# Kernel tuning notes

Measured on AMD Instinct MI355X. Metric: run time of the kernel, lower is better.

The kernel has to match this reference:

```python
import jax, jax.numpy as jnp
import numpy as np

# Dimensions
T = 1024      # tokens
D = 1024      # d_model
DFF = 1024    # expert intermediate dim
R = 64        # tucker rank (r_in == r_out)
G = 8         # n_group
E = 32        # experts_per_group
NEXP = G * E  # 256 routed experts
K = 8         # top-k


def setup_inputs() -> dict:
    key = jax.random.key(0)
    ks = jax.random.split(key, 12)
    s = 0.02
    return {
        "x": jax.random.normal(ks[0], (T, D), jnp.float32),
        "Wg": jax.random.normal(ks[1], (D, NEXP), jnp.float32) * s,
        "uin_gate": jax.random.normal(ks[2], (G, D, R), jnp.float32) * s,
        "core_gate": jax.random.normal(ks[3], (G, E, R, R), jnp.float32) * s,
        "uout_gate": jax.random.normal(ks[4], (G, R, DFF), jnp.float32) * s,
        "uin_up": jax.random.normal(ks[5], (G, D, R), jnp.float32) * s,
        "core_up": jax.random.normal(ks[6], (G, E, R, R), jnp.float32) * s,
        "uout_up": jax.random.normal(ks[7], (G, R, DFF), jnp.float32) * s,
        "uin_down": jax.random.normal(ks[8], (G, DFF, R), jnp.float32) * s,
        "core_down": jax.random.normal(ks[9], (G, E, R, R), jnp.float32) * s,
        "uout_down": jax.random.normal(ks[10], (G, R, D), jnp.float32) * s,
    }


def _moe_forward(x, Wg, uin_gate, core_gate, uout_gate,
                 uin_up, core_up, uout_up,
                 uin_down, core_down, uout_down):
    Tn, d = x.shape
    # Router: top-k over 256 experts, softmax over the k logits (fp32 as in torch)
    logits = x @ Wg                                   # [T, NEXP]
    w, sel = jax.lax.top_k(logits, K)                 # [T, K]
    w = jax.nn.softmax(w.astype(jnp.float32), axis=-1).astype(x.dtype)

    e = sel.reshape(-1)                               # [F] global expert id
    g = e // E                                        # [F] group id
    tok = jnp.repeat(jnp.arange(Tn), K)               # [F] source token id
    mask = (g[:, None] == jnp.arange(G)[None, :]).astype(x.dtype)  # [F, G]

    def gather_in(uin):
        # project tokens with every group's u_in once, then gather per pair
        pre = jnp.einsum('td,gdr->gtr', x, uin)       # [G, T, R]
        return pre[g, tok]                            # [F, R]

    def core_apply(xin, core):
        # per-pair Tucker core slice bmm: x.unsqueeze(1) @ core[rel_idx]
        slices = core.reshape(G * E, R, R)[e]         # [F, R, R] gather
        return jnp.einsum('fr,fro->fo', xin, slices)  # [F, R]

    def group_out(h, U):
        # per-pair group-specific projection: h[f] @ U[g_f]
        out = jnp.zeros((h.shape[0], U.shape[-1]), h.dtype)
        for gi in range(G):  # fixed small loop over 8 groups
            out = out + (h * mask[:, gi:gi + 1]) @ U[gi]
        return out

    gate_h = group_out(core_apply(gather_in(uin_gate), core_gate), uout_gate)  # [F, DFF]
    up_h = group_out(core_apply(gather_in(uin_up), core_up), uout_up)          # [F, DFF]
    act = jax.nn.silu(gate_h) * up_h                                           # SwiGLU
    xin_d = group_out(act, uin_down)                                           # [F, R]
    out_f = group_out(core_apply(xin_d, core_down), uout_down)                 # [F, D]
    out_f = out_f * w.reshape(-1)[:, None]
    # scatter-add expert outputs back to tokens
    return jax.ops.segment_sum(out_f, tok, num_segments=Tn)


def reference(x, Wg, uin_gate, core_gate, uout_gate,
              uin_up, core_up, uout_up,
              uin_down, core_down, uout_down):
    return _moe_forward(x, Wg, uin_gate, core_gate, uout_gate,
                        uin_up, core_up, uout_up,
                        uin_down, core_down, uout_down)
```

## Files before the change

### kernel.cpp

```cpp
#include <hip/hip_runtime.h>
#include <hip/hip_bf16.h>
#include <math.h>


#define T_ 1024
#define D_ 1024
#define DFF_ 1024
#define R_ 64
#define G_ 8
#define E_ 32
#define NEXP_ 256
#define K_ 8
#define F_ 8192
#define LKZ_ 8
#define LTB_ 8
#define PKZ_ 2
#define DKZ_ 4
#define LP_ 72

typedef short bf16x8 __attribute__((ext_vector_type(8)));
typedef float f32x4 __attribute__((ext_vector_type(4)));

__device__ __forceinline__ unsigned short f2bf(float f) {
  unsigned int u = __float_as_uint(f);
  u += 0x7fffu + ((u >> 16) & 1u);
  return (unsigned short)(u >> 16);
}
__device__ __forceinline__ float bf2f(unsigned short h) {
  return __uint_as_float((unsigned int)h << 16);
}

__device__ __forceinline__ void stage_tile(short* dst, const unsigned short* src,
                                           int gp, int tid) {
  for (int idx = tid; idx < 512; idx += 256) {
    int r = idx >> 3, c8 = (idx & 7) << 3;
    *(uint4*)&dst[r * LP_ + c8] = *(const uint4*)&src[(size_t)r * gp + c8];
  }
}

__device__ __forceinline__ void stage_tile_guard(short* dst, const unsigned short* src,
                                                 int gp, int rows_valid, int tid) {
  for (int idx = tid; idx < 512; idx += 256) {
    int r = idx >> 3, c8 = (idx & 7) << 3;
    uint4 v = make_uint4(0u, 0u, 0u, 0u);
    if (r < rows_valid) v = *(const uint4*)&src[(size_t)r * gp + c8];
    *(uint4*)&dst[r * LP_ + c8] = v;
  }
}

__device__ __forceinline__ void mma_strip(const short* As, const short* Bs,
                                          int ms, int lane, f32x4* acc) {
  int lm = lane & 15;
  int lk = (lane >> 4) << 3;
#pragma unroll
  for (int kc = 0; kc < 64; kc += 32) {
    bf16x8 a = *(const bf16x8*)&As[(ms + lm) * LP_ + kc + lk];
#pragma unroll
    for (int nt = 0; nt < 4; ++nt) {
      bf16x8 b = *(const bf16x8*)&Bs[(nt * 16 + lm) * LP_ + kc + lk];
      acc[nt] = __builtin_amdgcn_mfma_f32_16x16x32_bf16(a, b, acc[nt], 0, 0, 0);
    }
  }
}

__global__ __launch_bounds__(256) void k_prep_logits(
    const float* __restrict__ x, const float* __restrict__ Wg,
    const float* __restrict__ s0, const float* __restrict__ s1,
    const float* __restrict__ s2, const float* __restrict__ s3,
    const float* __restrict__ s4, const float* __restrict__ s5,
    unsigned short* __restrict__ xb,
    unsigned short* __restrict__ d0, unsigned short* __restrict__ d1,
    unsigned short* __restrict__ d2, unsigned short* __restrict__ d3,
    unsigned short* __restrict__ d4, unsigned short* __restrict__ d5,
    int* __restrict__ cnt, float* __restrict__ lp) {
  __shared__ float shbuf[64 * 65];
  int b = blockIdx.x;
  if (b < 896) {
    int id = b >> 7, rem = b & 127, g = rem >> 4, tile = rem & 15;
    if (id == 6) {
      size_t base = ((size_t)g * 16 + tile) * 8192;
      for (int i = threadIdx.x; i < 2048; i += 256) {
        size_t idx = base + (size_t)i * 4;
        float4 v = *(const float4*)&x[idx];
        xb[idx + 0] = f2bf(v.x);
        xb[idx + 1] = f2bf(v.y);
        xb[idx + 2] = f2bf(v.z);
        xb[idx + 3] = f2bf(v.w);
      }
      if (g == 0 && tile == 0) cnt[threadIdx.x] = 0;
      return;
    }
    const float* src = id == 0 ? s0 : id == 1 ? s1 : id == 2 ? s2 : id == 3 ? s3 : id == 4 ? s4 : s5;
    unsigned short* dst = id == 0 ? d0 : id == 1 ? d1 : id == 2 ? d2 : id == 3 ? d3 : id == 4 ? d4 : d5;
    if (id < 3) {
      int r0 = tile * 64;
      for (int idx = threadIdx.x; idx < 4096; idx += 256) {
        int r = idx >> 6, c = idx & 63;
        shbuf[r * 65 + c] = src[((size_t)g * 1024 + r0 + r) * 64 + c];
      }
      __syncthreads();
      for (int idx = threadIdx.x; idx < 4096; idx += 256) {
        int c = idx >> 6, r = idx & 63;
        dst[((size_t)g * 64 + c) * 1024 + r0 + r] = f2bf(shbuf[r * 65 + c]);
      }
    } else {
      int c0 = tile * 64;
      for (int idx = threadIdx.x; idx < 4096; idx += 256) {
        int r = idx >> 6, c = idx & 63;
        shbuf[r * 65 + c] = src[((size_t)g * 64 + r) * 1024 + c0 + c];
      }
      __syncthreads();
      if (id == 5) {
        for (int idx = threadIdx.x; idx < 4096; idx += 256) {
          int c = idx >> 6, r = idx & 63;
          dst[(size_t)(c0 + c) * 512 + g * 64 + r] = f2bf(shbuf[r * 65 + c]);
        }
      } else {
        for (int idx = threadIdx.x; idx < 4096; idx += 256) {
          int c = idx >> 6, r = idx & 63;
          dst[((size_t)g * 1024 + c0 + c) * 64 + r] = f2bf(shbuf[r * 65 + c]);
        }
      }
    }
    return;
  }
  int lb = b - 896;
  int t0 = (lb & 127) * LTB_;
  int z = lb >> 7;
  int e = threadIdx.x;
  float* xs = shbuf;
  float a[LTB_] = {};
  int dc = z * 128;
  {
    int idx = threadIdx.x * 4;
    int tl = idx >> 7, d = idx & 127;
    *(float4*)&xs[tl * 128 + d] = *(const float4*)&x[(size_t)(t0 + tl) * D_ + dc + d];
  }
  __syncthreads();
#pragma unroll 8
  for (int d2 = 0; d2 < 128; ++d2) {
    float wv = Wg[(size_t)(dc + d2) * NEXP_ + e];
#pragma unroll
    for (int j = 0; j < LTB_; ++j) a[j] = fmaf(xs[j * 128 + d2], wv, a[j]);
  }
  size_t base = (size_t)z * T_ * NEXP_;
#pragma unroll
  for (int j = 0; j < LTB_; ++j)
    lp[base + (size_t)(t0 + j) * NEXP_ + e] = a[j];
}

__global__ __launch_bounds__(256) void k_pre_topk(
    const unsigned short* __restrict__ xb,
    const unsigned short* __restrict__ uinT_g, const unsigned short* __restrict__ uinT_u,
    const float* __restrict__ lp,
    float* __restrict__ Pgp, float* __restrict__ Pup,
    int* __restrict__ sel, float* __restrict__ wsm, int* __restrict__ cnt) {
  __shared__ short sh2[2 * 64 * LP_];
  int b = blockIdx.x;
  if (b < 512) {
    int tile = b & 15, g = (b >> 4) & 7, zz = b >> 7;
    int gu = zz >> 1, kz = zz & 1;
    const unsigned short* U = gu ? uinT_u : uinT_g;
    float* P = gu ? Pup : Pgp;
    int t0 = tile * 64;
    short* As = sh2;
    short* Bs = sh2 + 64 * LP_;
    int tid = threadIdx.x, lane = tid & 63, ms = (tid >> 6) * 16;
    f32x4 acc[4] = {};
    int dlo = kz * (D_ / PKZ_);
    for (int dc = dlo; dc < dlo + D_ / PKZ_; dc += 64) {
      stage_tile(As, xb + (size_t)t0 * D_ + dc, D_, tid);
      stage_tile(Bs, U + (size_t)g * 64 * 1024 + dc, 1024, tid);
      __syncthreads();
      mma_strip(As, Bs, ms, lane, acc);
      __syncthreads();
    }
    int lm = lane & 15, lq = (lane >> 4) * 4;
#pragma unroll
    for (int nt = 0; nt < 4; ++nt)
#pragma unroll
      for (int r = 0; r < 4; ++r)
        P[((size_t)(kz * G_ + g) * T_ + t0 + ms + lq + r) * R_ + nt * 16 + lm] = acc[nt][r];
    return;
  }
  int tb = b - 512;
  int wave = threadIdx.x >> 6;
  int lane = threadIdx.x & 63;
  int t = tb * 4 + wave;
  float v[4];
  int idx[4];
#pragma unroll
  for (int j = 0; j < 4; ++j) {
    idx[j] = lane + 64 * j;
    float s = 0.f;
#pragma unroll
    for (int z = 0; z < LKZ_; ++z)
      s += lp[(size_t)z * T_ * NEXP_ + (size_t)t * NEXP_ + idx[j]];
    v[j] = s;
  }
  float topv[K_];
  int topi[K_];
#pragma unroll
  for (int k = 0; k < K_; ++k) {
    float bv = v[0];
    int bi = idx[0];
#pragma unroll
    for (int j = 1; j < 4; ++j)
      if (v[j] > bv || (v[j] == bv && idx[j] < bi)) { bv = v[j]; bi = idx[j]; }
#pragma unroll
    for (int off = 32; off > 0; off >>= 1) {
      float ov = __shfl_xor(bv, off);
      int oi = __shfl_xor(bi, off);
      if (ov > bv || (ov == bv && oi < bi)) { bv = ov; bi = oi; }
    }
    topv[k] = bv;
    topi[k] = bi;
#pragma unroll
    for (int j = 0; j < 4; ++j)
      if (idx[j] == bi) v[j] = -INFINITY;
  }
  float m = topv[0];
  float ev[K_];
  float s = 0.f;
#pragma unroll
  for (int k = 0; k < K_; ++k) { ev[k] = expf(topv[k] - m); s += ev[k]; }
  float inv = 1.f / s;
  if (lane < K_) {
    sel[t * K_ + lane] = topi[lane];
    wsm[t * K_ + lane] = ev[lane] * inv;
    atomicAdd(&cnt[topi[lane]], 1);
  }
}

__global__ __launch_bounds__(1024) void k_sortscan(const int* __restrict__ cnt,
                                                   const int* __restrict__ sel,
                                                   const float* __restrict__ wsm,
                                                   int* __restrict__ off,
                                                   int* __restrict__ stok,
                                                   int* __restrict__ se,
                                                   float* __restrict__ sw,
                                                   int* __restrict__ ipos) {
  __shared__ int s[NEXP_];
  __shared__ int offl[NEXP_];
  __shared__ int curl[NEXP_];
  int i = threadIdx.x;
  if (i < NEXP_) s[i] = cnt[i];
  __syncthreads();
  for (int d = 1; d < NEXP_; d <<= 1) {
    int v = 0;
    if (i < NEXP_ && i >= d) v = s[i - d];
    __syncthreads();
    if (i < NEXP_) s[i] += v;
    __syncthreads();
  }
  if (i < NEXP_) {
    offl[i] = s[i] - cnt[i];
    curl[i] = 0;
    off[i + 1] = s[i];
    if (i == 0) off[0] = 0;
  }
  __syncthreads();
  for (int f = i; f < F_; f += 1024) {
    int e = sel[f];
    int p = offl[e] + atomicAdd(&curl[e], 1);
    stok[p] = f >> 3;
    se[p] = e;
    sw[p] = wsm[f];
    ipos[f] = p;
  }
}

__global__ __launch_bounds__(256) void k_core_gu(const float* __restrict__ Pgp,
                                                 const float* __restrict__ Pup,
                                                 const float* __restrict__ core_g,
                                                 const float* __restrict__ core_u,
                                                 const int* __restrict__ stok,
                                                 const int* __restrict__ se,
                                                 unsigned short* __restrict__ xgb,
                                                 unsigned short* __restrict__ xub) {
  int pl = threadIdx.x >> 6;
  int o = threadIdx.x & 63;
  int p = blockIdx.x * 4 + pl;
  int e = se[p];
  int t = stok[p];
  int g = e >> 5;
  __shared__ float rg[4][64], ru[4][64];
  float sg = 0.f, su = 0.f;
#pragma unroll
  for (int kz = 0; kz < PKZ_; ++kz) {
    sg += Pgp[((size_t)(kz * G_ + g) * T_ + t) * R_ + o];
    su += Pup[((size_t)(kz * G_ + g) * T_ + t) * R_ + o];
  }
  rg[pl][o] = sg;
  ru[pl][o] = su;
  __syncthreads();
  const float* cg = core_g + (size_t)e * R_ * R_;
  const float* cu = core_u + (size_t)e * R_ * R_;
  float ag = 0.f, au = 0.f;
#pragma unroll 8
  for (int r = 0; r < R_; ++r) {
    ag = fmaf(rg[pl][r], cg[r * R_ + o], ag);
    au = fmaf(ru[pl][r], cu[r * R_ + o], au);
  }
  xgb[(size_t)p * R_ + o] = f2bf(ag);
  xub[(size_t)p * R_ + o] = f2bf(au);
}

__global__ __launch_bounds__(256) void k_fused_ad(const unsigned short* __restrict__ xgb,
                                                  const unsigned short* __restrict__ xub,
                                                  const unsigned short* __restrict__ uoutT_g,
                                                  const unsigned short* __restrict__ uoutT_u,
                                                  const unsigned short* __restrict__ uinT_d,
                                                  const int* __restrict__ off,
                                                  float* __restrict__ xdp) {
  int g = blockIdx.y;
  int kz = blockIdx.z;
  int p0 = off[g * E_];
  int pend = off[g * E_ + E_];
  int ntiles = (pend - p0 + 63) >> 6;
  __shared__ short Ag[64 * LP_], Au[64 * LP_];
  __shared__ short Bg[64 * LP_], Bu[64 * LP_], Bd[64 * LP_];
  __shared__ short Pt[64 * LP_];
  int tid = threadIdx.x, lane = tid & 63, ms = (tid >> 6) * 16;
  int lm = lane & 15, lq = (lane >> 4) * 4;
  for (int tile = blockIdx.x; tile < ntiles; tile += gridDim.x) {
    int pbase = p0 + tile * 64;
    int rv = pend - pbase; if (rv > 64) rv = 64;
    stage_tile_guard(Ag, xgb + (size_t)pbase * R_, R_, rv, tid);
    stage_tile_guard(Au, xub + (size_t)pbase * R_, R_, rv, tid);
    f32x4 accd[4] = {};
#pragma unroll
    for (int c4 = 0; c4 < 4; ++c4) {
      int cc = kz * (DFF_ / DKZ_) + c4 * 64;
      stage_tile(Bg, uoutT_g + ((size_t)g * DFF_ + cc) * R_, R_, tid);
      stage_tile(Bu, uoutT_u + ((size_t)g * DFF_ + cc) * R_, R_, tid);
      stage_tile(Bd, uinT_d + (size_t)g * 64 * 1024 + cc, 1024, tid);
      __syncthreads();
      f32x4 accg[4] = {}, accu[4] = {};
      mma_strip(Ag, Bg, ms, lane, accg);
      mma_strip(Au, Bu, ms, lane, accu);
#pragma unroll
      for (int nt = 0; nt < 4; ++nt)
#pragma unroll
        for (int r = 0; r < 4; ++r) {
          float gv = accg[nt][r];
          float av = gv / (1.f + expf(-gv)) * accu[nt][r];
          Pt[(ms + lq + r) * LP_ + nt * 16 + lm] = (short)f2bf(av);
        }
      mma_strip(Pt, Bd, ms, lane, accd);
      __syncthreads();
    }
#pragma unroll
    for (int nt = 0; nt < 4; ++nt)
#pragma unroll
      for (int r = 0; r < 4; ++r) {
        int p = pbase + ms + lq + r;
        if (p < pend) xdp[((size_t)kz * F_ + p) * R_ + nt * 16 + lm] = accd[nt][r];
      }
    __syncthreads();
  }
}

__global__ __launch_bounds__(256) void k_core_down(const float* __restrict__ xdp,
                                                   const float* __restrict__ core_d,
                                                   const int* __restrict__ se,
                                                   unsigned short* __restrict__ xd2b) {
  int pl = threadIdx.x >> 6;
  int o = threadIdx.x & 63;
  int p = blockIdx.x * 4 + pl;
  int e = se[p];
  __shared__ float rg[4][64];
  float s = 0.f;
#pragma unroll
  for (int kz = 0; kz < DKZ_; ++kz) s += xdp[((size_t)kz * F_ + p) * R_ + o];
  rg[pl][o] = s;
  __syncthreads();
  const float* cd = core_d + (size_t)e * R_ * R_;
  float a = 0.f;
#pragma unroll 8
  for (int r = 0; r < R_; ++r) a = fmaf(rg[pl][r], cd[r * R_ + o], a);
  xd2b[(size_t)p * R_ + o] = f2bf(a);
}

__global__ __launch_bounds__(256) void k_accY(const unsigned short* __restrict__ xd2b,
                                              const int* __restrict__ ipos,
                                              const int* __restrict__ se,
                                              const float* __restrict__ sw,
                                              unsigned short* __restrict__ Ybf) {
  int t = blockIdx.x * 4 + (threadIdx.x >> 6);
  int o = threadIdx.x & 63;
  float y[G_] = {};
#pragma unroll
  for (int k = 0; k < K_; ++k) {
    int p = ipos[t * K_ + k];
    int g = se[p] >> 5;
    y[g] += sw[p] * bf2f(xd2b[(size_t)p * R_ + o]);
  }
#pragma unroll
  for (int g = 0; g < G_; ++g)
    Ybf[(size_t)t * 512 + g * 64 + o] = f2bf(y[g]);
}

__global__ __launch_bounds__(256) void k_fin(const unsigned short* __restrict__ Ybf,
                                             const unsigned short* __restrict__ Uod2T,
                                             float* __restrict__ out) {
  int t0 = blockIdx.x * 64;
  int d0 = blockIdx.y * 64;
  __shared__ short As[64 * LP_], Bs[64 * LP_];
  __shared__ float Os[64 * 68];
  int tid = threadIdx.x, lane = tid & 63, ms = (tid >> 6) * 16;
  int lm = lane & 15, lq = (lane >> 4) * 4;
  f32x4 acc[4] = {};
  for (int kc = 0; kc < 512; kc += 64) {
    stage_tile(As, Ybf + (size_t)t0 * 512 + kc, 512, tid);
    stage_tile(Bs, Uod2T + (size_t)d0 * 512 + kc, 512, tid);
    __syncthreads();
    mma_strip(As, Bs, ms, lane, acc);
    __syncthreads();
  }
#pragma unroll
  for (int nt = 0; nt < 4; ++nt)
#pragma unroll
    for (int r = 0; r < 4; ++r)
      Os[(ms + lq + r) * 68 + nt * 16 + lm] = acc[nt][r];
  __syncthreads();
  for (int idx = tid; idx < 1024; idx += 256) {
    int r = idx >> 4, c4 = (idx & 15) << 2;
    *(float4*)&out[(size_t)(t0 + r) * D_ + d0 + c4] = *(const float4*)&Os[r * 68 + c4];
  }
}

extern "C" void kernel_launch(void* const* d_in, const int* in_sizes, int n_in,
                              void* d_out, int out_size, void* d_ws, size_t ws_size,
                              hipStream_t stream) {
  const float* x = (const float*)d_in[0];
  const float* Wg = (const float*)d_in[1];
  const float* uin_gate = (const float*)d_in[2];
  const float* core_gate = (const float*)d_in[3];
  const float* uout_gate = (const float*)d_in[4];
  const float* uin_up = (const float*)d_in[5];
  const float* core_up = (const float*)d_in[6];
  const float* uout_up = (const float*)d_in[7];
  const float* uin_down = (const float*)d_in[8];
  const float* core_down = (const float*)d_in[9];
  const float* uout_down = (const float*)d_in[10];
  float* out = (float*)d_out;

  char* ws = (char*)d_ws;
  size_t o = 0;
  auto alloc = [&](size_t bytes) { size_t r = o; o = (o + bytes + 255) & ~(size_t)255; return r; };
  size_t o_lp = alloc((size_t)LKZ_ * T_ * NEXP_ * 4);
  size_t o_sel = alloc(F_ * 4);
  size_t o_wsm = alloc(F_ * 4);
  size_t o_cnt = alloc(NEXP_ * 4);
  size_t o_off = alloc((NEXP_ + 1) * 4);
  size_t o_stok = alloc(F_ * 4);
  size_t o_se = alloc(F_ * 4);
  size_t o_sw = alloc(F_ * 4);
  size_t o_ipos = alloc(F_ * 4);
  size_t o_xb = alloc((size_t)T_ * D_ * 2);
  size_t o_uinT_g = alloc((size_t)G_ * 64 * 1024 * 2);
  size_t o_uinT_u = alloc((size_t)G_ * 64 * 1024 * 2);
  size_t o_uinT_d = alloc((size_t)G_ * 64 * 1024 * 2);
  size_t o_uoutT_g = alloc((size_t)G_ * 1024 * 64 * 2);
  size_t o_uoutT_u = alloc((size_t)G_ * 1024 * 64 * 2);
  size_t o_Uod2T = alloc((size_t)D_ * 512 * 2);
  size_t o_xgb = alloc((size_t)F_ * R_ * 2);
  size_t o_xub = alloc((size_t)F_ * R_ * 2);
  size_t o_xd2b = alloc((size_t)F_ * R_ * 2);
  size_t o_Y = alloc((size_t)T_ * 512 * 2);
  size_t o_pgp = alloc((size_t)PKZ_ * G_ * T_ * R_ * 4);
  size_t o_pup = alloc((size_t)PKZ_ * G_ * T_ * R_ * 4);
  size_t o_xdp = alloc((size_t)DKZ_ * F_ * R_ * 4);
  (void)ws_size;

  float* lp = (float*)(ws + o_lp);
  int* sel = (int*)(ws + o_sel);
  float* wsm = (float*)(ws + o_wsm);
  int* cnt = (int*)(ws + o_cnt);
  int* off = (int*)(ws + o_off);
  int* stok = (int*)(ws + o_stok);
  int* se = (int*)(ws + o_se);
  float* sw = (float*)(ws + o_sw);
  int* ipos = (int*)(ws + o_ipos);
  unsigned short* xb = (unsigned short*)(ws + o_xb);
  unsigned short* uinT_g = (unsigned short*)(ws + o_uinT_g);
  unsigned short* uinT_u = (unsigned short*)(ws + o_uinT_u);
  unsigned short* uinT_d = (unsigned short*)(ws + o_uinT_d);
  unsigned short* uoutT_g = (unsigned short*)(ws + o_uoutT_g);
  unsigned short* uoutT_u = (unsigned short*)(ws + o_uoutT_u);
  unsigned short* Uod2T = (unsigned short*)(ws + o_Uod2T);
  unsigned short* xgb = (unsigned short*)(ws + o_xgb);
  unsigned short* xub = (unsigned short*)(ws + o_xub);
  unsigned short* xd2b = (unsigned short*)(ws + o_xd2b);
  unsigned short* Ybf = (unsigned short*)(ws + o_Y);
  float* pgp = (float*)(ws + o_pgp);
  float* pup = (float*)(ws + o_pup);
  float* xdp = (float*)(ws + o_xdp);

  k_prep_logits<<<1920, 256, 0, stream>>>(x, Wg, uin_gate, uin_up, uin_down,
                                          uout_gate, uout_up, uout_down, xb,
                                          uinT_g, uinT_u, uinT_d,
                                          uoutT_g, uoutT_u, Uod2T, cnt, lp);
  k_pre_topk<<<768, 256, 0, stream>>>(xb, uinT_g, uinT_u, lp, pgp, pup, sel, wsm, cnt);
  k_sortscan<<<1, 1024, 0, stream>>>(cnt, sel, wsm, off, stok, se, sw, ipos);
  k_core_gu<<<F_ / 4, 256, 0, stream>>>(pgp, pup, core_gate, core_up, stok, se, xgb, xub);
  k_fused_ad<<<dim3(16, G_, DKZ_), 256, 0, stream>>>(xgb, xub, uoutT_g, uoutT_u, uinT_d, off, xdp);
  k_core_down<<<F_ / 4, 256, 0, stream>>>(xdp, core_down, se, xd2b);
  k_accY<<<T_ / 4, 256, 0, stream>>>(xd2b, ipos, se, sw, Ybf);
  k_fin<<<dim3(16, 16), 256, 0, stream>>>(Ybf, Uod2T, out);
}
```

Before: 221.2 us.

## Compute sorted positions from topk atomics and fuse core_down with token accumulation

The top-k kernel now keeps the return value of its per-expert atomic counter as a rank. The single-block sort/scatter kernel shrinks to a 256-thread prefix scan, and later kernels compute each pair's sorted position as off[e]+rank[f] in place of reading scattered index arrays. The core_down and accY kernels are merged into one per-token kernel that applies the core slice, weights by the softmax and reduces across the 8 pairs in shared memory. This drops one launch, the serial scatter loop and the bf16 round trip through xd2b. The trade-offs are that atomic order makes the sorted order nondeterministic, and the fused kernel runs only 1024 blocks with extra barriers.

```diff
diff --git a/kernel.cpp b/kernel.cpp
--- a/kernel.cpp
+++ b/kernel.cpp
@@ -25,9 +25,6 @@
   unsigned int u = __float_as_uint(f);
   u += 0x7fffu + ((u >> 16) & 1u);
   return (unsigned short)(u >> 16);
-}
-__device__ __forceinline__ float bf2f(unsigned short h) {
-  return __uint_as_float((unsigned int)h << 16);
 }
 
 __device__ __forceinline__ void stage_tile(short* dst, const unsigned short* src,
@@ -154,7 +151,8 @@
     const unsigned short* __restrict__ uinT_g, const unsigned short* __restrict__ uinT_u,
     const float* __restrict__ lp,
     float* __restrict__ Pgp, float* __restrict__ Pup,
-    int* __restrict__ sel, float* __restrict__ wsm, int* __restrict__ cnt) {
+    int* __restrict__ sel, float* __restrict__ wsm,
+    int* __restrict__ rank, int* __restrict__ cnt) {
   __shared__ short sh2[2 * 64 * LP_];
   int b = blockIdx.x;
   if (b < 512) {
@@ -228,62 +226,42 @@
   if (lane < K_) {
     sel[t * K_ + lane] = topi[lane];
     wsm[t * K_ + lane] = ev[lane] * inv;
-    atomicAdd(&cnt[topi[lane]], 1);
-  }
-}
-
-__global__ __launch_bounds__(1024) void k_sortscan(const int* __restrict__ cnt,
-                                                   const int* __restrict__ sel,
-                                                   const float* __restrict__ wsm,
-                                                   int* __restrict__ off,
-                                                   int* __restrict__ stok,
-                                                   int* __restrict__ se,
-                                                   float* __restrict__ sw,
-                                                   int* __restrict__ ipos) {
+    rank[t * K_ + lane] = atomicAdd(&cnt[topi[lane]], 1);
+  }
+}
+
+__global__ __launch_bounds__(256) void k_scan(const int* __restrict__ cnt,
+                                              int* __restrict__ off) {
   __shared__ int s[NEXP_];
-  __shared__ int offl[NEXP_];
-  __shared__ int curl[NEXP_];
   int i = threadIdx.x;
-  if (i < NEXP_) s[i] = cnt[i];
+  s[i] = cnt[i];
   __syncthreads();
   for (int d = 1; d < NEXP_; d <<= 1) {
-    int v = 0;
-    if (i < NEXP_ && i >= d) v = s[i - d];
-    __syncthreads();
-    if (i < NEXP_) s[i] += v;
-    __syncthreads();
-  }
-  if (i < NEXP_) {
-    offl[i] = s[i] - cnt[i];
-    curl[i] = 0;
-    off[i + 1] = s[i];
-    if (i == 0) off[0] = 0;
-  }
-  __syncthreads();
-  for (int f = i; f < F_; f += 1024) {
-    int e = sel[f];
-    int p = offl[e] + atomicAdd(&curl[e], 1);
-    stok[p] = f >> 3;
-    se[p] = e;
-    sw[p] = wsm[f];
-    ipos[f] = p;
-  }
+    int v = (i >= d) ? s[i - d] : 0;
+    __syncthreads();
+    s[i] += v;
+    __syncthreads();
+  }
+  off[i + 1] = s[i];
+  if (i == 0) off[0] = 0;
 }
 
 __global__ __launch_bounds__(256) void k_core_gu(const float* __restrict__ Pgp,
                                                  const float* __restrict__ Pup,
                                                  const float* __restrict__ core_g,
                                                  const float* __restrict__ core_u,
-                                                 const int* __restrict__ stok,
-                                                 const int* __restrict__ se,
+                                                 const int* __restrict__ sel,
+                                                 const int* __restrict__ rank,
+                                                 const int* __restrict__ off,
                                                  unsigned short* __restrict__ xgb,
                                                  unsigned short* __restrict__ xub) {
   int pl = threadIdx.x >> 6;
   int o = threadIdx.x & 63;
-  int p = blockIdx.x * 4 + pl;
-  int e = se[p];
-  int t = stok[p];
+  int f = blockIdx.x * 4 + pl;
+  int t = f >> 3;
+  int e = sel[f];
   int g = e >> 5;
+  int p = off[e] + rank[f];
   __shared__ float rg[4][64], ru[4][64];
   float sg = 0.f, su = 0.f;
 #pragma unroll
@@ -361,44 +339,44 @@
   }
 }
 
-__global__ __launch_bounds__(256) void k_core_down(const float* __restrict__ xdp,
+__global__ __launch_bounds__(256) void k_down_accY(const float* __restrict__ xdp,
                                                    const float* __restrict__ core_d,
-                                                   const int* __restrict__ se,
-                                                   unsigned short* __restrict__ xd2b) {
-  int pl = threadIdx.x >> 6;
-  int o = threadIdx.x & 63;
-  int p = blockIdx.x * 4 + pl;
-  int e = se[p];
-  __shared__ float rg[4][64];
-  float s = 0.f;
-#pragma unroll
-  for (int kz = 0; kz < DKZ_; ++kz) s += xdp[((size_t)kz * F_ + p) * R_ + o];
-  rg[pl][o] = s;
+                                                   const int* __restrict__ sel,
+                                                   const int* __restrict__ rank,
+                                                   const float* __restrict__ wsm,
+                                                   const int* __restrict__ off,
+                                                   unsigned short* __restrict__ Ybf) {
+  int t = blockIdx.x;
+  int w = threadIdx.x >> 6, o = threadIdx.x & 63;
+  __shared__ float xs[4][64];
+  __shared__ float yl[4][G_][64];
+  float y[G_] = {};
+#pragma unroll
+  for (int kk = 0; kk < 2; ++kk) {
+    int f = t * K_ + w * 2 + kk;
+    int e = sel[f];
+    int g = e >> 5;
+    int p = off[e] + rank[f];
+    float s = 0.f;
+#pragma unroll
+    for (int kz = 0; kz < DKZ_; ++kz) s += xdp[((size_t)kz * F_ + p) * R_ + o];
+    __syncthreads();
+    xs[w][o] = s;
+    __syncthreads();
+    const float* cd = core_d + (size_t)e * R_ * R_;
+    float a = 0.f;
+#pragma unroll 8
+    for (int r = 0; r < R_; ++r) a = fmaf(xs[w][r], cd[r * R_ + o], a);
+    y[g] += wsm[f] * a;
+  }
+#pragma unroll
+  for (int g = 0; g < G_; ++g) yl[w][g][o] = y[g];
   __syncthreads();
-  const float* cd = core_d + (size_t)e * R_ * R_;
-  float a = 0.f;
-#pragma unroll 8
-  for (int r = 0; r < R_; ++r) a = fmaf(rg[pl][r], cd[r * R_ + o], a);
-  xd2b[(size_t)p * R_ + o] = f2bf(a);
-}
-
-__global__ __launch_bounds__(256) void k_accY(const unsigned short* __restrict__ xd2b,
-                                              const int* __restrict__ ipos,
-                                              const int* __restrict__ se,
-                                              const float* __restrict__ sw,
-                                              unsigned short* __restrict__ Ybf) {
-  int t = blockIdx.x * 4 + (threadIdx.x >> 6);
-  int o = threadIdx.x & 63;
-  float y[G_] = {};
-#pragma unroll
-  for (int k = 0; k < K_; ++k) {
-    int p = ipos[t * K_ + k];
-    int g = se[p] >> 5;
-    y[g] += sw[p] * bf2f(xd2b[(size_t)p * R_ + o]);
-  }
-#pragma unroll
-  for (int g = 0; g < G_; ++g)
-    Ybf[(size_t)t * 512 + g * 64 + o] = f2bf(y[g]);
+  for (int idx = threadIdx.x; idx < 512; idx += 256) {
+    int g = idx >> 6, oo = idx & 63;
+    float v = yl[0][g][oo] + yl[1][g][oo] + yl[2][g][oo] + yl[3][g][oo];
+    Ybf[(size_t)t * 512 + g * 64 + oo] = f2bf(v);
+  }
 }
 
 __global__ __launch_bounds__(256) void k_fin(const unsigned short* __restrict__ Ybf,
@@ -452,12 +430,9 @@
   size_t o_lp = alloc((size_t)LKZ_ * T_ * NEXP_ * 4);
   size_t o_sel = alloc(F_ * 4);
   size_t o_wsm = alloc(F_ * 4);
+  size_t o_rank = alloc(F_ * 4);
   size_t o_cnt = alloc(NEXP_ * 4);
   size_t o_off = alloc((NEXP_ + 1) * 4);
-  size_t o_stok = alloc(F_ * 4);
-  size_t o_se = alloc(F_ * 4);
-  size_t o_sw = alloc(F_ * 4);
-  size_t o_ipos = alloc(F_ * 4);
   size_t o_xb = alloc((size_t)T_ * D_ * 2);
   size_t o_uinT_g = alloc((size_t)G_ * 64 * 1024 * 2);
   size_t o_uinT_u = alloc((size_t)G_ * 64 * 1024 * 2);
@@ -467,7 +442,6 @@
   size_t o_Uod2T = alloc((size_t)D_ * 512 * 2);
   size_t o_xgb = alloc((size_t)F_ * R_ * 2);
   size_t o_xub = alloc((size_t)F_ * R_ * 2);
-  size_t o_xd2b = alloc((size_t)F_ * R_ * 2);
   size_t o_Y = alloc((size_t)T_ * 512 * 2);
   size_t o_pgp = alloc((size_t)PKZ_ * G_ * T_ * R_ * 4);
   size_t o_pup = alloc((size_t)PKZ_ * G_ * T_ * R_ * 4);
@@ -477,12 +451,9 @@
   float* lp = (float*)(ws + o_lp);
   int* sel = (int*)(ws + o_sel);
   float* wsm = (float*)(ws + o_wsm);
+  int* rank = (int*)(ws + o_rank);
   int* cnt = (int*)(ws + o_cnt);
   int* off = (int*)(ws + o_off);
-  int* stok = (int*)(ws + o_stok);
-  int* se = (int*)(ws + o_se);
-  float* sw = (float*)(ws + o_sw);
-  int* ipos = (int*)(ws + o_ipos);
   unsigned short* xb = (unsigned short*)(ws + o_xb);
   unsigned short* uinT_g = (unsigned short*)(ws + o_uinT_g);
   unsigned short* uinT_u = (unsigned short*)(ws + o_uinT_u);
@@ -492,7 +463,6 @@
   unsigned short* Uod2T = (unsigned short*)(ws + o_Uod2T);
   unsigned short* xgb = (unsigned short*)(ws + o_xgb);
   unsigned short* xub = (unsigned short*)(ws + o_xub);
-  unsigned short* xd2b = (unsigned short*)(ws + o_xd2b);
   unsigned short* Ybf = (unsigned short*)(ws + o_Y);
   float* pgp = (float*)(ws + o_pgp);
   float* pup = (float*)(ws + o_pup);
@@ -502,11 +472,10 @@
                                           uout_gate, uout_up, uout_down, xb,
                                           uinT_g, uinT_u, uinT_d,
                                           uoutT_g, uoutT_u, Uod2T, cnt, lp);
-  k_pre_topk<<<768, 256, 0, stream>>>(xb, uinT_g, uinT_u, lp, pgp, pup, sel, wsm, cnt);
-  k_sortscan<<<1, 1024, 0, stream>>>(cnt, sel, wsm, off, stok, se, sw, ipos);
-  k_core_gu<<<F_ / 4, 256, 0, stream>>>(pgp, pup, core_gate, core_up, stok, se, xgb, xub);
+  k_pre_topk<<<768, 256, 0, stream>>>(xb, uinT_g, uinT_u, lp, pgp, pup, sel, wsm, rank, cnt);
+  k_scan<<<1, 256, 0, stream>>>(cnt, off);
+  k_core_gu<<<F_ / 4, 256, 0, stream>>>(pgp, pup, core_gate, core_up, sel, rank, off, xgb, xub);
   k_fused_ad<<<dim3(16, G_, DKZ_), 256, 0, stream>>>(xgb, xub, uoutT_g, uoutT_u, uinT_d, off, xdp);
-  k_core_down<<<F_ / 4, 256, 0, stream>>>(xdp, core_down, se, xd2b);
-  k_accY<<<T_ / 4, 256, 0, stream>>>(xd2b, ipos, se, sw, Ybf);
+  k_down_accY<<<T_, 256, 0, stream>>>(xdp, core_down, sel, rank, wsm, off, Ybf);
   k_fin<<<dim3(16, 16), 256, 0, stream>>>(Ybf, Uod2T, out);
 }
```

Measured after the change: 201.9 us. 1.1x faster.
